# Kernel tuning notes

Hardware: AMD Instinct MI355X
Metric: run time of the kernel (lower is better)

## Reference

```python
import jax, jax.numpy as jnp
import numpy as np

STRIDES = (8, 16, 32, 64, 128)
THRESHOLD = 0.5
B, C = 8, 80
HS = (160, 80, 40, 20, 10)


def setup_inputs() -> dict:
    key = jax.random.key(0)
    ks = jax.random.split(key, 3 * len(HS))
    d = {}
    for i, h in enumerate(HS):
        d[f"cls_{i}"] = jax.random.normal(ks[3 * i], (B, C, h, h), jnp.float32)
        d[f"bbox_{i}"] = jax.random.normal(ks[3 * i + 1], (B, 4, h, h), jnp.float32)
        d[f"ctr_{i}"] = jax.random.normal(ks[3 * i + 2], (B, 1, h, h), jnp.float32)
    return d


def _filter_level(cls, bbox, ctr, stride, thr):
    # cls: [B,C,H,W], bbox: [B,4,H,W], ctr: [B,1,H,W] (NCHW, as asserted in source)
    b, c, h, w = cls.shape
    scores = cls.transpose(0, 2, 3, 1).reshape(b, h * w, c)   # [B,HW,C]
    bboxes = bbox.transpose(0, 2, 3, 1).reshape(b, h * w, 4)  # [B,HW,4]
    ctrs = ctr.transpose(0, 2, 3, 1).reshape(b, h * w, 1)     # [B,HW,1]
    # FilterModule keeps locations whose max class score exceeds threshold.
    mask = (jnp.max(scores, axis=-1) > thr)[..., None].astype(scores.dtype)  # [B,HW,1]
    ys, xs = jnp.meshgrid(jnp.arange(h), jnp.arange(w), indexing="ij")
    half = stride // 2
    coord = jnp.stack([xs * stride + half, ys * stride + half], axis=-1)  # [H,W,2]
    coord = coord.reshape(h * w, 2).astype(scores.dtype)
    coord = jnp.broadcast_to(coord, (b, h * w, 2))
    # Static-shape compaction: zero out non-selected locations instead of
    # producing dynamic-length per-image lists (jit-compatible equivalent of
    # the per-image coord/score/bbox/centerness gather).
    return jnp.concatenate(
        [coord * mask, scores * mask, bboxes * mask, ctrs * mask], axis=-1
    )  # [B, HW, 2 + C + 4 + 1]


def reference(cls_0, bbox_0, ctr_0, cls_1, bbox_1, ctr_1, cls_2, bbox_2, ctr_2,
              cls_3, bbox_3, ctr_3, cls_4, bbox_4, ctr_4):
    levels = [
        (cls_0, bbox_0, ctr_0),
        (cls_1, bbox_1, ctr_1),
        (cls_2, bbox_2, ctr_2),
        (cls_3, bbox_3, ctr_3),
        (cls_4, bbox_4, ctr_4),
    ]
    return tuple(
        _filter_level(c, bb, ct, s, THRESHOLD)
        for (c, bb, ct), s in zip(levels, STRIDES)
    )
```

## Files before the change

kernel.cpp:

```cpp
#include <hip/hip_runtime.h>

#define NCH   85
#define TILE  64
#define LS    67
#define OUTCH 87

__global__ __launch_bounds__(256) void fcos_filter_kernel(
    const float* __restrict__ c0, const float* __restrict__ b0, const float* __restrict__ t0,
    const float* __restrict__ c1, const float* __restrict__ b1, const float* __restrict__ t1,
    const float* __restrict__ c2, const float* __restrict__ b2, const float* __restrict__ t2,
    const float* __restrict__ c3, const float* __restrict__ b3, const float* __restrict__ t3,
    const float* __restrict__ c4, const float* __restrict__ b4, const float* __restrict__ t4,
    float* __restrict__ out)
{
    __shared__ float lds[NCH * LS];
    __shared__ float s_flag[TILE];

    const int bid = blockIdx.x;
    const int tid = threadIdx.x;

    const float *cls, *bbx, *ctr;
    int img, tile, HW, W, str, ksh;
    size_t obase;
    if (bid < 3200)      { cls=c0; bbx=b0; ctr=t0; HW=25600; W=160; str=8;   ksh=4; obase=0u;
                           img = bid / 400;          tile = bid - img * 400; }
    else if (bid < 4000) { cls=c1; bbx=b1; ctr=t1; HW=6400;  W=80;  str=16;  ksh=3; obase=17817600u;
                           const int bl = bid - 3200; img = bl / 100; tile = bl - img * 100; }
    else if (bid < 4200) { cls=c2; bbx=b2; ctr=t2; HW=1600;  W=40;  str=32;  ksh=2; obase=22272000u;
                           const int bl = bid - 4000; img = bl / 25;  tile = bl - img * 25; }
    else if (bid < 4256) { cls=c3; bbx=b3; ctr=t3; HW=400;   W=20;  str=64;  ksh=1; obase=23385600u;
                           const int bl = bid - 4200; img = bl / 7;   tile = bl - img * 7; }
    else                 { cls=c4; bbx=b4; ctr=t4; HW=100;   W=10;  str=128; ksh=0; obase=23664000u;
                           const int bl = bid - 4256; img = bl >> 1;  tile = bl & 1; }

    const int p0    = tile * TILE;
    const int valid = min(TILE, HW - p0);

    if (tid < TILE) s_flag[tid] = 0.0f;
    __syncthreads();

    const int  lane_c = tid >> 4;
    const int  q4     = (tid & 15) << 2;
    const bool qok    = q4 < valid;

    float4 v0, v1, v2, v3, v4, v5;
    const float* abase = cls + ((size_t)img * 80 + lane_c) * HW + p0 + q4;
    if (qok) {
        v0 = *reinterpret_cast<const float4*>(abase);
        v1 = *reinterpret_cast<const float4*>(abase + (size_t)16 * HW);
        v2 = *reinterpret_cast<const float4*>(abase + (size_t)32 * HW);
        v3 = *reinterpret_cast<const float4*>(abase + (size_t)48 * HW);
        v4 = *reinterpret_cast<const float4*>(abase + (size_t)64 * HW);
    }
    const bool r5 = (tid < 80) && qok;
    if (r5) {
        const float* s5 = (lane_c < 4)
            ? bbx + ((size_t)img * 4 + lane_c) * HW + p0 + q4
            : ctr + (size_t)img * HW + p0 + q4;
        v5 = *reinterpret_cast<const float4*>(s5);
    }

    #define PUT(base_c, V, FLAGS)                                   \
    {   const int a = (base_c + lane_c) * LS + q4;                  \
        lds[a + 0] = V.x; lds[a + 1] = V.y;                         \
        lds[a + 2] = V.z; lds[a + 3] = V.w;                         \
        if (FLAGS) {                                                \
            if (V.x > 0.5f) s_flag[q4 + 0] = 1.0f;                  \
            if (V.y > 0.5f) s_flag[q4 + 1] = 1.0f;                  \
            if (V.z > 0.5f) s_flag[q4 + 2] = 1.0f;                  \
            if (V.w > 0.5f) s_flag[q4 + 3] = 1.0f;                  \
        }                                                           \
    }

    if (qok) {
        PUT(0,  v0, true) PUT(16, v1, true) PUT(32, v2, true)
        PUT(48, v3, true) PUT(64, v4, true)
    }
    if (r5) { PUT(80, v5, false) }
    #undef PUT

    __syncthreads();

    float* dst = out + obase + ((size_t)img * HW + p0) * OUTCH;
    #pragma unroll 4
    for (int e = tid; e < TILE * OUTCH; e += 256) {
        const int p  = e / OUTCH;
        if (p >= valid) break;
        const int ch = e - p * OUTCH;
        const float m = s_flag[p];
        float val;
        if (ch >= 2) {
            val = lds[(ch - 2) * LS + p] * m;
        } else {
            const int pg = p0 + p;
            const int t  = pg >> ksh;
            const int y  = t / 10;
            const int x  = pg - y * W;
            const int coord = (ch == 0) ? x : y;
            val = (float)(coord * str + (str >> 1)) * m;
        }
        __builtin_nontemporal_store(val, dst + e);
    }
}

extern "C" void kernel_launch(void* const* d_in, const int* in_sizes, int n_in,
                              void* d_out, int out_size, void* d_ws, size_t ws_size,
                              hipStream_t stream) {
    (void)in_sizes; (void)n_in; (void)out_size; (void)d_ws; (void)ws_size;
    fcos_filter_kernel<<<4272, 256, 0, stream>>>(
        (const float*)d_in[0],  (const float*)d_in[1],  (const float*)d_in[2],
        (const float*)d_in[3],  (const float*)d_in[4],  (const float*)d_in[5],
        (const float*)d_in[6],  (const float*)d_in[7],  (const float*)d_in[8],
        (const float*)d_in[9],  (const float*)d_in[10], (const float*)d_in[11],
        (const float*)d_in[12], (const float*)d_in[13], (const float*)d_in[14],
        (float*)d_out);
}
```

Baseline: 35.25 us.

## Vectorize output stores to float4 and compute class-max mask via wave shuffles

Result: no change. 35.48 us (+0.7%).

```diff
diff --git a/kernel.cpp b/kernel.cpp
--- a/kernel.cpp
+++ b/kernel.cpp
@@ -4,6 +4,9 @@
 #define TILE  64
 #define LS    67
 #define OUTCH 87
+#define NF4   1392
+
+typedef float f32x4 __attribute__((ext_vector_type(4)));
 
 __global__ __launch_bounds__(256) void fcos_filter_kernel(
     const float* __restrict__ c0, const float* __restrict__ b0, const float* __restrict__ t0,
@@ -36,14 +39,12 @@
     const int p0    = tile * TILE;
     const int valid = min(TILE, HW - p0);
 
-    if (tid < TILE) s_flag[tid] = 0.0f;
-    __syncthreads();
-
     const int  lane_c = tid >> 4;
     const int  q4     = (tid & 15) << 2;
     const bool qok    = q4 < valid;
 
     float4 v0, v1, v2, v3, v4, v5;
+    float4 fm = make_float4(-1e30f, -1e30f, -1e30f, -1e30f);
     const float* abase = cls + ((size_t)img * 80 + lane_c) * HW + p0 + q4;
     if (qok) {
         v0 = *reinterpret_cast<const float4*>(abase);
@@ -51,6 +52,10 @@
         v2 = *reinterpret_cast<const float4*>(abase + (size_t)32 * HW);
         v3 = *reinterpret_cast<const float4*>(abase + (size_t)48 * HW);
         v4 = *reinterpret_cast<const float4*>(abase + (size_t)64 * HW);
+        fm.x = fmaxf(fmaxf(fmaxf(v0.x, v1.x), fmaxf(v2.x, v3.x)), v4.x);
+        fm.y = fmaxf(fmaxf(fmaxf(v0.y, v1.y), fmaxf(v2.y, v3.y)), v4.y);
+        fm.z = fmaxf(fmaxf(fmaxf(v0.z, v1.z), fmaxf(v2.z, v3.z)), v4.z);
+        fm.w = fmaxf(fmaxf(fmaxf(v0.w, v1.w), fmaxf(v2.w, v3.w)), v4.w);
     }
     const bool r5 = (tid < 80) && qok;
     if (r5) {
@@ -60,46 +65,72 @@
         v5 = *reinterpret_cast<const float4*>(s5);
     }
 
-    #define PUT(base_c, V, FLAGS)                                   \
+    #define PUT(base_c, V)                                          \
     {   const int a = (base_c + lane_c) * LS + q4;                  \
         lds[a + 0] = V.x; lds[a + 1] = V.y;                         \
         lds[a + 2] = V.z; lds[a + 3] = V.w;                         \
-        if (FLAGS) {                                                \
-            if (V.x > 0.5f) s_flag[q4 + 0] = 1.0f;                  \
-            if (V.y > 0.5f) s_flag[q4 + 1] = 1.0f;                  \
-            if (V.z > 0.5f) s_flag[q4 + 2] = 1.0f;                  \
-            if (V.w > 0.5f) s_flag[q4 + 3] = 1.0f;                  \
-        }                                                           \
     }
-
-    if (qok) {
-        PUT(0,  v0, true) PUT(16, v1, true) PUT(32, v2, true)
-        PUT(48, v3, true) PUT(64, v4, true)
-    }
-    if (r5) { PUT(80, v5, false) }
+    if (qok) { PUT(0, v0) PUT(16, v1) PUT(32, v2) PUT(48, v3) PUT(64, v4) }
+    if (r5)  { PUT(80, v5) }
     #undef PUT
 
+    fm.x = fmaxf(fm.x, __shfl_xor(fm.x, 16));
+    fm.y = fmaxf(fm.y, __shfl_xor(fm.y, 16));
+    fm.z = fmaxf(fm.z, __shfl_xor(fm.z, 16));
+    fm.w = fmaxf(fm.w, __shfl_xor(fm.w, 16));
+    fm.x = fmaxf(fm.x, __shfl_xor(fm.x, 32));
+    fm.y = fmaxf(fm.y, __shfl_xor(fm.y, 32));
+    fm.z = fmaxf(fm.z, __shfl_xor(fm.z, 32));
+    fm.w = fmaxf(fm.w, __shfl_xor(fm.w, 32));
+
+    if (tid < TILE) s_flag[tid] = 0.0f;
+    __syncthreads();
+
+    if ((tid & 63) < 16) {
+        if (fm.x > 0.5f) s_flag[q4 + 0] = 1.0f;
+        if (fm.y > 0.5f) s_flag[q4 + 1] = 1.0f;
+        if (fm.z > 0.5f) s_flag[q4 + 2] = 1.0f;
+        if (fm.w > 0.5f) s_flag[q4 + 3] = 1.0f;
+    }
     __syncthreads();
 
     float* dst = out + obase + ((size_t)img * HW + p0) * OUTCH;
-    #pragma unroll 4
-    for (int e = tid; e < TILE * OUTCH; e += 256) {
-        const int p  = e / OUTCH;
-        if (p >= valid) break;
-        const int ch = e - p * OUTCH;
-        const float m = s_flag[p];
-        float val;
-        if (ch >= 2) {
-            val = lds[(ch - 2) * LS + p] * m;
+    const int nmax = valid * OUTCH;
+    #pragma unroll
+    for (int r = 0; r < 6; ++r) {
+        const int f4 = tid + 256 * r;
+        if (r == 5 && f4 >= NF4) break;
+        const int e0 = f4 * 4;
+        if (e0 >= nmax) break;
+        const int p  = e0 / OUTCH;
+        const int ch = e0 - p * OUTCH;
+        float vals[4];
+        #pragma unroll
+        for (int j = 0; j < 4; ++j) {
+            int chj = ch + j, pj = p;
+            if (chj >= OUTCH) { chj -= OUTCH; pj += 1; }
+            const float m = s_flag[pj];
+            float val;
+            if (chj >= 2) {
+                val = lds[(chj - 2) * LS + pj] * m;
+            } else {
+                const int pg = p0 + pj;
+                const int t  = pg >> ksh;
+                const int y  = t / 10;
+                const int x  = pg - y * W;
+                const int coord = (chj == 0) ? x : y;
+                val = (float)(coord * str + (str >> 1)) * m;
+            }
+            vals[j] = val;
+        }
+        if (e0 + 4 <= nmax) {
+            f32x4 o; o.x = vals[0]; o.y = vals[1]; o.z = vals[2]; o.w = vals[3];
+            __builtin_nontemporal_store(o, reinterpret_cast<f32x4*>(dst + e0));
         } else {
-            const int pg = p0 + p;
-            const int t  = pg >> ksh;
-            const int y  = t / 10;
-            const int x  = pg - y * W;
-            const int coord = (ch == 0) ? x : y;
-            val = (float)(coord * str + (str >> 1)) * m;
+            #pragma unroll
+            for (int j = 0; j < 4; ++j)
+                if (e0 + j < nmax) __builtin_nontemporal_store(vals[j], dst + e0 + j);
         }
-        __builtin_nontemporal_store(val, dst + e);
     }
 }
 
```
